# Kernel tuning notes

Measured on AMD Instinct MI355X. Metric: run time of the kernel, lower is better.

## Reference

```python
import jax, jax.numpy as jnp
import numpy as np

N_NODES = 100000
N_EDGES = 1200000
D_IN = 64
D_HID = 64
BN_EPS = 1e-5


def setup_inputs() -> dict:
    key = jax.random.key(0)
    ks = jax.random.split(key, 16)
    x = jax.random.normal(ks[0], (N_NODES, D_IN), dtype=jnp.float32)
    edge_index = jax.random.randint(ks[1], (2, N_EDGES), 0, N_NODES, dtype=jnp.int64)
    s = 1.0 / np.sqrt(D_HID)
    W1 = jax.random.uniform(ks[2], (D_IN, D_HID), jnp.float32, -s, s)
    b1 = jax.random.uniform(ks[3], (D_HID,), jnp.float32, -s, s)
    W2 = jax.random.uniform(ks[4], (D_HID, D_HID), jnp.float32, -s, s)
    b2 = jax.random.uniform(ks[5], (D_HID,), jnp.float32, -s, s)
    W3 = jax.random.uniform(ks[6], (D_HID, D_HID), jnp.float32, -s, s)
    b3 = jax.random.uniform(ks[7], (D_HID,), jnp.float32, -s, s)
    gamma1 = jnp.ones((D_HID,), jnp.float32)
    beta1 = jnp.zeros((D_HID,), jnp.float32)
    gamma2 = jnp.ones((D_HID,), jnp.float32)
    beta2 = jnp.zeros((D_HID,), jnp.float32)
    return {"x": x, "edge_index": edge_index, "batch_size": 1,
            "W1": W1, "b1": b1, "gamma1": gamma1, "beta1": beta1,
            "W2": W2, "b2": b2, "gamma2": gamma2, "beta2": beta2,
            "W3": W3, "b3": b3}


def _gcn_norm(edge_index, n):
    # PyG GCNConv: add self-loops, symmetric normalization D^-1/2 (A+I) D^-1/2
    loop = jnp.arange(n, dtype=edge_index.dtype)
    src = jnp.concatenate([edge_index[0], loop])
    dst = jnp.concatenate([edge_index[1], loop])
    deg = jax.ops.segment_sum(jnp.ones_like(dst, dtype=jnp.float32), dst, num_segments=n)
    dinv = jnp.where(deg > 0, jax.lax.rsqrt(jnp.maximum(deg, 1.0)), 0.0)
    norm = dinv[src] * dinv[dst]  # [E + N]
    return src, dst, norm


def _gcn_conv(h, W, b, src, dst, norm, n):
    h = h @ W                      # [N, D]
    msg = h[src] * norm[:, None]   # gather + scale, [E+N, D]
    out = jax.ops.segment_sum(msg, dst, num_segments=n)  # scatter-add
    return out + b


def _bn_train(h, gamma, beta):
    # BatchNorm1d over nodes, training-mode (biased batch statistics)
    m = h.mean(axis=0)
    v = h.var(axis=0)
    return (h - m) * jax.lax.rsqrt(v + BN_EPS) * gamma + beta


def reference(x, edge_index, batch_size,
              W1, b1, gamma1, beta1, W2, b2, gamma2, beta2, W3, b3):
    n = x.shape[0]
    src, dst, norm = _gcn_norm(edge_index, n)
    h = _gcn_conv(x, W1, b1, src, dst, norm, n)
    h = jax.nn.relu(_bn_train(h, gamma1, beta1))
    h = _gcn_conv(h, W2, b2, src, dst, norm, n)
    h = jax.nn.relu(_bn_train(h, gamma2, beta2))
    h = _gcn_conv(h, W3, b3, src, dst, norm, n)
    return h  # output_type == 'hidden'
```

## Files before the change

### kernel.cpp

```cpp
#include <hip/hip_runtime.h>
#include <hip/hip_bf16.h>

#define D 64

typedef __attribute__((ext_vector_type(8))) short bf16x8;
typedef __attribute__((ext_vector_type(8))) unsigned short u16x8;
typedef __attribute__((ext_vector_type(4))) float f32x4;

__device__ __forceinline__ short f2bf(float x) {
    unsigned u = __float_as_uint(x);
    unsigned r = (u + 0x7fffu + ((u >> 16) & 1u)) >> 16;
    return (short)r;
}
__device__ __forceinline__ float bf2f(unsigned short u) {
    return __uint_as_float((unsigned)u << 16);
}

__global__ void detect_kernel(const unsigned int* e32, int* flag) {
    __shared__ int nz;
    if (threadIdx.x == 0) nz = 0;
    __syncthreads();
    if (e32[2 * threadIdx.x + 1] != 0) nz = 1;
    __syncthreads();
    if (threadIdx.x == 0) *flag = (nz == 0) ? 1 : 0;
}

__device__ __forceinline__ int load_idx(const void* e, int is64, long long i) {
    if (is64) return (int)((const long long*)e)[i];
    return ((const int*)e)[i];
}

#define NBLK 256

__global__ __launch_bounds__(256) void bucket_count_kernel(
    const void* edges, const int* flag, int* pbh, int E, int shift) {
    __shared__ int h[512];
    for (int i = threadIdx.x; i < 512; i += 256) h[i] = 0;
    __syncthreads();
    int is64 = *flag;
    int chunk = (E + gridDim.x - 1) / gridDim.x;
    int s0 = blockIdx.x * chunk;
    int s1 = min(E, s0 + chunk);
    for (int e = s0 + (int)threadIdx.x; e < s1; e += 256) {
        int d = load_idx(edges, is64, (long long)E + e);
        atomicAdd(&h[d >> shift], 1);
    }
    __syncthreads();
    for (int i = threadIdx.x; i < 512; i += 256) pbh[blockIdx.x * 512 + i] = h[i];
}

__global__ __launch_bounds__(256) void colscan_kernel(int* pbh, int* btot) {
    int b = blockIdx.x;
    int k = threadIdx.x;
    __shared__ int sA[256], sB[256];
    int v = pbh[k * 512 + b];
    sA[k] = v;
    __syncthreads();
    int* src = sA;
    int* dst = sB;
    for (int d = 1; d < 256; d <<= 1) {
        dst[k] = src[k] + (k >= d ? src[k - d] : 0);
        __syncthreads();
        int* t = src; src = dst; dst = t;
    }
    pbh[k * 512 + b] = src[k] - v;
    if (k == 255) btot[b] = src[255];
}

__global__ __launch_bounds__(512) void basescan_kernel(const int* btot, int* bbase, int E) {
    __shared__ int sA[512], sB[512];
    int b = threadIdx.x;
    int v = btot[b];
    sA[b] = v;
    __syncthreads();
    int* src = sA;
    int* dst = sB;
    for (int d = 1; d < 512; d <<= 1) {
        dst[b] = src[b] + (b >= d ? src[b - d] : 0);
        __syncthreads();
        int* t = src; src = dst; dst = t;
    }
    bbase[b] = src[b] - v;
    if (b == 0) bbase[512] = E;
}

__global__ __launch_bounds__(256) void bucket_scatter_kernel(
    const void* edges, const int* flag, const int* pbh, const int* bbase,
    unsigned* staging, int E, int shift) {
    __shared__ int cur[512];
    for (int i = threadIdx.x; i < 512; i += 256)
        cur[i] = pbh[blockIdx.x * 512 + i] + bbase[i];
    __syncthreads();
    int is64 = *flag;
    int chunk = (E + gridDim.x - 1) / gridDim.x;
    int s0 = blockIdx.x * chunk;
    int s1 = min(E, s0 + chunk);
    unsigned mask = (unsigned)((1 << shift) - 1);
    for (int e = s0 + (int)threadIdx.x; e < s1; e += 256) {
        int s = load_idx(edges, is64, e);
        int d = load_idx(edges, is64, (long long)E + e);
        int b = d >> shift;
        int pos = atomicAdd(&cur[b], 1);
        staging[pos] = ((unsigned)s << shift) | ((unsigned)d & mask);
    }
}

__global__ __launch_bounds__(256) void bucket_fill_kernel(
    const unsigned* __restrict__ staging, const int* __restrict__ bbase,
    int* __restrict__ offs, float* __restrict__ dinv, int* __restrict__ srcs,
    int shift, int n, int E) {
    int b = blockIdx.x;
    int bstart = bbase[b], bend = bbase[b + 1];
    int bsz = 1 << shift;
    unsigned mask = (unsigned)(bsz - 1);
    int v0 = b << shift;
    int nloc = min(bsz, n - v0);

    __shared__ int cnt[512], cur[512], sA[512], sB[512];
    for (int i = threadIdx.x; i < bsz; i += 256) cnt[i] = 0;
    __syncthreads();
    for (int idx = bstart + (int)threadIdx.x; idx < bend; idx += 256)
        atomicAdd(&cnt[staging[idx] & mask], 1);
    __syncthreads();
    for (int i = threadIdx.x; i < bsz; i += 256) sA[i] = cnt[i];
    __syncthreads();
    int* src = sA;
    int* dst = sB;
    for (int d = 1; d < bsz; d <<= 1) {
        for (int i = threadIdx.x; i < bsz; i += 256)
            dst[i] = src[i] + (i >= d ? src[i - d] : 0);
        __syncthreads();
        int* t = src; src = dst; dst = t;
    }
    for (int i = threadIdx.x; i < bsz; i += 256) {
        int excl = src[i] - cnt[i];
        cur[i] = excl;
        if (i < nloc) {
            offs[v0 + i] = bstart + excl;
            dinv[v0 + i] = rsqrtf((float)(cnt[i] + 1));
        }
    }
    if (b == 0 && threadIdx.x == 0) offs[n] = E;
    __syncthreads();
    for (int idx = bstart + (int)threadIdx.x; idx < bend; idx += 256) {
        unsigned u = staging[idx];
        int ld = (int)(u & mask);
        int pos = atomicAdd(&cur[ld], 1);
        srcs[bstart + pos] = (int)(u >> shift);
    }
}

__global__ __launch_bounds__(256) void mm_bn_kernel(
    const float* __restrict__ Xf, const unsigned short* __restrict__ Xb, int x_is_bf16,
    const float* __restrict__ W,
    const float* __restrict__ stats, const float* __restrict__ gamma,
    const float* __restrict__ beta, int use_bn, float inv_n,
    const float* __restrict__ dinv,
    unsigned short* __restrict__ Y, int n) {
    int lane = threadIdx.x & 63;
    int m = lane & 15;
    int quad = lane >> 4;

    float sc[16], sh[16];
#pragma unroll
    for (int s = 0; s < 2; s++) {
#pragma unroll
        for (int j = 0; j < 8; j++) {
            float scale = 1.f, shift = 0.f;
            if (use_bn) {
                int f = s * 32 + quad * 8 + j;
                float mean = stats[f] * inv_n;
                float var = stats[64 + f] * inv_n - mean * mean;
                float rs = rsqrtf(var + 1e-5f);
                scale = rs * gamma[f];
                shift = beta[f] - mean * scale;
            }
            sc[s * 8 + j] = scale;
            sh[s * 8 + j] = shift;
        }
    }

    bf16x8 bfrag[4][2];
#pragma unroll
    for (int nt = 0; nt < 4; nt++) {
#pragma unroll
        for (int s = 0; s < 2; s++) {
#pragma unroll
            for (int j = 0; j < 8; j++) {
                int k = s * 32 + quad * 8 + j;
                bfrag[nt][s][j] = f2bf(W[k * 64 + nt * 16 + m]);
            }
        }
    }

    int wave = blockIdx.x * 4 + (threadIdx.x >> 6);
    int nwaves = gridDim.x * 4;
    int ntiles = (n + 15) >> 4;
    const f32x4 zero = {0.f, 0.f, 0.f, 0.f};

    for (int t = wave; t < ntiles; t += nwaves) {
        int r = t * 16 + m;
        if (r >= n) r = n - 1;
        float av[16];
        if (x_is_bf16) {
            const unsigned short* xr = Xb + (long long)r * 64;
            u16x8 u0 = *(const u16x8*)(xr + quad * 8);
            u16x8 u1 = *(const u16x8*)(xr + 32 + quad * 8);
#pragma unroll
            for (int j = 0; j < 8; j++) {
                av[j] = bf2f(u0[j]);
                av[8 + j] = bf2f(u1[j]);
            }
        } else {
            const float* xr = Xf + (long long)r * 64;
            f32x4 a0 = *(const f32x4*)(xr + quad * 8);
            f32x4 a1 = *(const f32x4*)(xr + quad * 8 + 4);
            f32x4 a2 = *(const f32x4*)(xr + 32 + quad * 8);
            f32x4 a3 = *(const f32x4*)(xr + 32 + quad * 8 + 4);
#pragma unroll
            for (int j = 0; j < 4; j++) {
                av[j] = a0[j];
                av[4 + j] = a1[j];
                av[8 + j] = a2[j];
                av[12 + j] = a3[j];
            }
        }
        bf16x8 A0, A1;
#pragma unroll
        for (int j = 0; j < 8; j++) {
            float v0 = av[j] * sc[j] + sh[j];
            float v1 = av[8 + j] * sc[8 + j] + sh[8 + j];
            if (use_bn) {
                v0 = fmaxf(v0, 0.f);
                v1 = fmaxf(v1, 0.f);
            }
            A0[j] = f2bf(v0);
            A1[j] = f2bf(v1);
        }

        f32x4 acc[4];
#pragma unroll
        for (int nt = 0; nt < 4; nt++) {
            acc[nt] = __builtin_amdgcn_mfma_f32_16x16x32_bf16(A0, bfrag[nt][0], zero, 0, 0, 0);
            acc[nt] = __builtin_amdgcn_mfma_f32_16x16x32_bf16(A1, bfrag[nt][1], acc[nt], 0, 0, 0);
        }

        int row0 = t * 16 + quad * 4;
        float dv[4];
#pragma unroll
        for (int i = 0; i < 4; i++) {
            int rr = row0 + i;
            dv[i] = (rr < n) ? dinv[rr] : 0.f;
        }
#pragma unroll
        for (int nt = 0; nt < 4; nt++) {
#pragma unroll
            for (int i = 0; i < 4; i++) {
                int rr = row0 + i;
                if (rr < n)
                    Y[(long long)rr * 64 + nt * 16 + m] = (unsigned short)f2bf(acc[nt][i] * dv[i]);
            }
        }
    }
}

__global__ __launch_bounds__(256) void agg_kernel(
    const unsigned short* __restrict__ T,
    const int* __restrict__ offs,
    const int* __restrict__ srcs,
    const float* __restrict__ dinv,
    const float* __restrict__ bias,
    unsigned short* __restrict__ out16,
    float* __restrict__ out32, int out_bf16,
    float* __restrict__ stats, int do_stats,
    int n, int E) {
    __shared__ float S[128];
    if (do_stats) {
        if (threadIdx.x < 128) S[threadIdx.x] = 0.f;
        __syncthreads();
    }
    int lane = threadIdx.x & 63;
    int sub = lane >> 3;
    int c = lane & 7;
    int wave = blockIdx.x * 4 + (threadIdx.x >> 6);
    int nwaves = gridDim.x * 4;
    int ngrp = (n + 7) >> 3;
    f32x4 bi0 = *(const f32x4*)(bias + c * 8);
    f32x4 bi1 = *(const f32x4*)(bias + c * 8 + 4);
    float ss[8], sq[8];
#pragma unroll
    for (int i = 0; i < 8; i++) { ss[i] = 0.f; sq[i] = 0.f; }

    for (int g = wave; g < ngrp; g += nwaves) {
        int v = g * 8 + sub;
        int valid = v < n;
        int vc = valid ? v : n - 1;
        int j0 = offs[vc];
        int len = offs[vc + 1] - j0;
        u16x8 sv = *(const u16x8*)(T + ((size_t)(unsigned)vc << 6) + (c << 3));
        float acc[8];
#pragma unroll
        for (int i = 0; i < 8; i++) acc[i] = bf2f(sv[i]);
        int ml = len;
        ml = max(ml, __shfl_xor(ml, 8));
        ml = max(ml, __shfl_xor(ml, 16));
        ml = max(ml, __shfl_xor(ml, 32));
        for (int base = 0; base < ml; base += 8) {
            int my = srcs[min(j0 + base + c, E - 1)];
            int lim = min(8, ml - base);
            int rel = len - base;
            for (int e = 0; e < lim; e += 4) {
                int sid[4];
                float w[4];
#pragma unroll
                for (int u = 0; u < 4; u++) {
                    int ee = e + u;
                    int s = __shfl(my, (lane & 56) | ee);
                    int live = ee < rel;
                    sid[u] = live ? s : vc;
                    w[u] = live ? 1.f : 0.f;
                }
                u16x8 r[4];
#pragma unroll
                for (int u = 0; u < 4; u++)
                    r[u] = *(const u16x8*)(T + ((size_t)(unsigned)sid[u] << 6) + (c << 3));
#pragma unroll
                for (int u = 0; u < 4; u++) {
#pragma unroll
                    for (int i = 0; i < 8; i++)
                        acc[i] += w[u] * bf2f(r[u][i]);
                }
            }
        }
        float dv = dinv[vc];
        float val[8];
#pragma unroll
        for (int i = 0; i < 4; i++) {
            val[i] = dv * acc[i] + bi0[i];
            val[4 + i] = dv * acc[4 + i] + bi1[i];
        }
        if (valid) {
            if (out_bf16) {
                u16x8 o;
#pragma unroll
                for (int i = 0; i < 8; i++) o[i] = (unsigned short)f2bf(val[i]);
                *(u16x8*)(out16 + ((size_t)(unsigned)v << 6) + (c << 3)) = o;
            } else {
                f32x4 o0 = {val[0], val[1], val[2], val[3]};
                f32x4 o1 = {val[4], val[5], val[6], val[7]};
                float* op = out32 + ((size_t)(unsigned)v << 6) + (c << 3);
                *(f32x4*)op = o0;
                *(f32x4*)(op + 4) = o1;
            }
            if (do_stats) {
#pragma unroll
                for (int i = 0; i < 8; i++) {
                    ss[i] += val[i];
                    sq[i] += val[i] * val[i];
                }
            }
        }
    }
    if (do_stats) {
#pragma unroll
        for (int i = 0; i < 8; i++) {
            atomicAdd(&S[c * 8 + i], ss[i]);
            atomicAdd(&S[64 + c * 8 + i], sq[i]);
        }
        __syncthreads();
        if (threadIdx.x < 128) atomicAdd(&stats[threadIdx.x], S[threadIdx.x]);
    }
}

extern "C" void kernel_launch(void* const* d_in, const int* in_sizes, int n_in,
                              void* d_out, int out_size, void* d_ws, size_t ws_size,
                              hipStream_t stream) {
    const float* x = (const float*)d_in[0];
    const void* edges = d_in[1];
    const float* W1 = (const float*)d_in[3];
    const float* b1 = (const float*)d_in[4];
    const float* gamma1 = (const float*)d_in[5];
    const float* beta1 = (const float*)d_in[6];
    const float* W2 = (const float*)d_in[7];
    const float* b2 = (const float*)d_in[8];
    const float* gamma2 = (const float*)d_in[9];
    const float* beta2 = (const float*)d_in[10];
    const float* W3 = (const float*)d_in[11];
    const float* b3 = (const float*)d_in[12];

    const int N = in_sizes[0] / D;
    const int E = in_sizes[1] / 2;
    const float inv_n = 1.f / (float)N;

    int shift = 8;
    while ((((long long)N - 1) >> shift) + 1 > 512) shift++;
    const int nbuk = (int)(((long long)N - 1) >> shift) + 1;

    char* ws = (char*)d_ws;
    size_t off = 0;
    auto alloc = [&](size_t bytes) -> void* {
        void* p = ws + off;
        off = (off + bytes + 255) & ~(size_t)255;
        return p;
    };
    float*    dinv    = (float*)   alloc((size_t)N * 4);
    int*      offs    = (int*)     alloc((size_t)(N + 1) * 4);
    int*      srcs    = (int*)     alloc((size_t)E * 4);
    unsigned* staging = (unsigned*)alloc((size_t)E * 4);
    int*      pbh     = (int*)     alloc((size_t)NBLK * 512 * 4);
    int*      btot    = (int*)     alloc(512 * 4);
    int*      bbase   = (int*)     alloc(513 * 4);
    int*      flag    = (int*)     alloc(4);
    float*    stats   = (float*)   alloc(256 * 4);
    unsigned short* bufA = (unsigned short*)alloc((size_t)N * D * 2);
    unsigned short* hbuf = (unsigned short*)alloc((size_t)N * D * 2);
    float*    outf    = (float*)d_out;

    const int AGGB = 1536;
    const int MMB  = 782;

    detect_kernel<<<1, 256, 0, stream>>>((const unsigned int*)edges, flag);
    bucket_count_kernel<<<NBLK, 256, 0, stream>>>(edges, flag, pbh, E, shift);
    colscan_kernel<<<512, 256, 0, stream>>>(pbh, btot);
    basescan_kernel<<<1, 512, 0, stream>>>(btot, bbase, E);
    bucket_scatter_kernel<<<NBLK, 256, 0, stream>>>(edges, flag, pbh, bbase, staging, E, shift);
    bucket_fill_kernel<<<nbuk, 256, 0, stream>>>(staging, bbase, offs, dinv, srcs, shift, N, E);
    hipMemsetAsync(stats, 0, 256 * 4, stream);

    mm_bn_kernel<<<MMB, 256, 0, stream>>>(x, nullptr, 0, W1, nullptr, nullptr, nullptr, 0,
                                          inv_n, dinv, bufA, N);
    agg_kernel<<<AGGB, 256, 0, stream>>>(bufA, offs, srcs, dinv, b1, hbuf, nullptr, 1,
                                         stats, 1, N, E);

    mm_bn_kernel<<<MMB, 256, 0, stream>>>(nullptr, hbuf, 1, W2, stats, gamma1, beta1, 1,
                                          inv_n, dinv, bufA, N);
    agg_kernel<<<AGGB, 256, 0, stream>>>(bufA, offs, srcs, dinv, b2, hbuf, nullptr, 1,
                                         stats + 128, 1, N, E);

    mm_bn_kernel<<<MMB, 256, 0, stream>>>(nullptr, hbuf, 1, W3, stats + 128, gamma2, beta2, 1,
                                          inv_n, dinv, bufA, N);
    agg_kernel<<<AGGB, 256, 0, stream>>>(bufA, offs, srcs, dinv, b3, nullptr, outf, 0,
                                         nullptr, 0, N, E);
}
```

Baseline: 360.6 us.

## Sort nodes by degree so aggregation waves process uniform-length neighbor lists

Adds a counting sort of nodes by in-degree (histogram, column scan, base scan, scatter) that produces a permutation with per-node edge offsets and lengths. The aggregation kernel walks nodes in that order, so the eight nodes sharing a wave have similar degrees and less work is lost to divergence. Each lane now loads its own source indices directly, eight at a time, instead of broadcasting them with shuffles. In exchange there are four extra preprocessing launches and the output writes land at scattered, permuted rows.

```diff
diff --git a/kernel.cpp b/kernel.cpp
--- a/kernel.cpp
+++ b/kernel.cpp
@@ -150,6 +150,79 @@
     }
 }
 
+#define DBIN 256
+
+__global__ __launch_bounds__(256) void deg_count_kernel(
+    const int* __restrict__ offs, int* __restrict__ pdh, int n) {
+    __shared__ int h[DBIN];
+    for (int i = threadIdx.x; i < DBIN; i += 256) h[i] = 0;
+    __syncthreads();
+    int chunk = (n + gridDim.x - 1) / gridDim.x;
+    int s0 = blockIdx.x * chunk;
+    int s1 = min(n, s0 + chunk);
+    for (int v = s0 + (int)threadIdx.x; v < s1; v += 256) {
+        int d = min(offs[v + 1] - offs[v], DBIN - 1);
+        atomicAdd(&h[d], 1);
+    }
+    __syncthreads();
+    for (int i = threadIdx.x; i < DBIN; i += 256) pdh[blockIdx.x * DBIN + i] = h[i];
+}
+
+__global__ __launch_bounds__(256) void deg_colscan_kernel(int* pdh, int* dtot) {
+    int b = blockIdx.x;
+    int k = threadIdx.x;
+    __shared__ int sA[256], sB[256];
+    int v = pdh[k * DBIN + b];
+    sA[k] = v;
+    __syncthreads();
+    int* src = sA;
+    int* dst = sB;
+    for (int d = 1; d < 256; d <<= 1) {
+        dst[k] = src[k] + (k >= d ? src[k - d] : 0);
+        __syncthreads();
+        int* t = src; src = dst; dst = t;
+    }
+    pdh[k * DBIN + b] = src[k] - v;
+    if (k == 255) dtot[b] = src[255];
+}
+
+__global__ __launch_bounds__(256) void deg_base_kernel(const int* dtot, int* dbase) {
+    __shared__ int sA[256], sB[256];
+    int b = threadIdx.x;
+    int v = dtot[b];
+    sA[b] = v;
+    __syncthreads();
+    int* src = sA;
+    int* dst = sB;
+    for (int d = 1; d < 256; d <<= 1) {
+        dst[b] = src[b] + (b >= d ? src[b - d] : 0);
+        __syncthreads();
+        int* t = src; src = dst; dst = t;
+    }
+    dbase[b] = src[b] - v;
+}
+
+__global__ __launch_bounds__(256) void deg_scatter_kernel(
+    const int* __restrict__ offs, const int* __restrict__ pdh, const int* __restrict__ dbase,
+    int* __restrict__ perm, int* __restrict__ pj0, int* __restrict__ plen, int n) {
+    __shared__ int cur[DBIN];
+    for (int i = threadIdx.x; i < DBIN; i += 256)
+        cur[i] = pdh[blockIdx.x * DBIN + i] + dbase[i];
+    __syncthreads();
+    int chunk = (n + gridDim.x - 1) / gridDim.x;
+    int s0 = blockIdx.x * chunk;
+    int s1 = min(n, s0 + chunk);
+    for (int v = s0 + (int)threadIdx.x; v < s1; v += 256) {
+        int a = offs[v];
+        int d = offs[v + 1] - a;
+        int bin = min(d, DBIN - 1);
+        int pos = atomicAdd(&cur[bin], 1);
+        perm[pos] = v;
+        pj0[pos] = a;
+        plen[pos] = d;
+    }
+}
+
 __global__ __launch_bounds__(256) void mm_bn_kernel(
     const float* __restrict__ Xf, const unsigned short* __restrict__ Xb, int x_is_bf16,
     const float* __restrict__ W,
@@ -266,14 +339,16 @@
 
 __global__ __launch_bounds__(256) void agg_kernel(
     const unsigned short* __restrict__ T,
-    const int* __restrict__ offs,
+    const int* __restrict__ perm,
+    const int* __restrict__ pj0,
+    const int* __restrict__ plen,
     const int* __restrict__ srcs,
     const float* __restrict__ dinv,
     const float* __restrict__ bias,
     unsigned short* __restrict__ out16,
     float* __restrict__ out32, int out_bf16,
     float* __restrict__ stats, int do_stats,
-    int n, int E) {
+    int n) {
     __shared__ float S[128];
     if (do_stats) {
         if (threadIdx.x < 128) S[threadIdx.x] = 0.f;
@@ -291,81 +366,93 @@
 #pragma unroll
     for (int i = 0; i < 8; i++) { ss[i] = 0.f; sq[i] = 0.f; }
 
+    const char* Tb = (const char*)T;
+    unsigned coff = (unsigned)c << 4;
+
     for (int g = wave; g < ngrp; g += nwaves) {
-        int v = g * 8 + sub;
-        int valid = v < n;
-        int vc = valid ? v : n - 1;
-        int j0 = offs[vc];
-        int len = offs[vc + 1] - j0;
-        u16x8 sv = *(const u16x8*)(T + ((size_t)(unsigned)vc << 6) + (c << 3));
+        int i = g * 8 + sub;
+        int valid = i < n;
+        int ic = valid ? i : n - 1;
+        int v = perm[ic];
+        int j0 = pj0[ic];
+        int len = plen[ic];
+        u16x8 sv = *(const u16x8*)(Tb + (((unsigned)v << 7) + coff));
         float acc[8];
 #pragma unroll
-        for (int i = 0; i < 8; i++) acc[i] = bf2f(sv[i]);
-        int ml = len;
-        ml = max(ml, __shfl_xor(ml, 8));
-        ml = max(ml, __shfl_xor(ml, 16));
-        ml = max(ml, __shfl_xor(ml, 32));
-        for (int base = 0; base < ml; base += 8) {
-            int my = srcs[min(j0 + base + c, E - 1)];
-            int lim = min(8, ml - base);
-            int rel = len - base;
-            for (int e = 0; e < lim; e += 4) {
-                int sid[4];
-                float w[4];
-#pragma unroll
-                for (int u = 0; u < 4; u++) {
-                    int ee = e + u;
-                    int s = __shfl(my, (lane & 56) | ee);
-                    int live = ee < rel;
-                    sid[u] = live ? s : vc;
-                    w[u] = live ? 1.f : 0.f;
-                }
-                u16x8 r[4];
-#pragma unroll
-                for (int u = 0; u < 4; u++)
-                    r[u] = *(const u16x8*)(T + ((size_t)(unsigned)sid[u] << 6) + (c << 3));
-#pragma unroll
-                for (int u = 0; u < 4; u++) {
-#pragma unroll
-                    for (int i = 0; i < 8; i++)
-                        acc[i] += w[u] * bf2f(r[u][i]);
-                }
-            }
-        }
-        float dv = dinv[vc];
+        for (int q = 0; q < 8; q++) acc[q] = bf2f(sv[q]);
+
+        int j = j0, j1 = j0 + len;
+        for (; j + 8 <= j1; j += 8) {
+            int sid[8];
+#pragma unroll
+            for (int u = 0; u < 8; u++) sid[u] = srcs[j + u];
+            u16x8 r[8];
+#pragma unroll
+            for (int u = 0; u < 8; u++)
+                r[u] = *(const u16x8*)(Tb + (((unsigned)sid[u] << 7) + coff));
+#pragma unroll
+            for (int u = 0; u < 8; u++) {
+#pragma unroll
+                for (int q = 0; q < 8; q++) acc[q] += bf2f(r[u][q]);
+            }
+        }
+        if (j < j1) {
+            int sid[8];
+            float w[8];
+#pragma unroll
+            for (int u = 0; u < 8; u++) {
+                int jj = j + u;
+                int live = jj < j1;
+                int jc = live ? jj : j1 - 1;
+                int s = srcs[jc];
+                sid[u] = live ? s : v;
+                w[u] = live ? 1.f : 0.f;
+            }
+            u16x8 r[8];
+#pragma unroll
+            for (int u = 0; u < 8; u++)
+                r[u] = *(const u16x8*)(Tb + (((unsigned)sid[u] << 7) + coff));
+#pragma unroll
+            for (int u = 0; u < 8; u++) {
+#pragma unroll
+                for (int q = 0; q < 8; q++) acc[q] += w[u] * bf2f(r[u][q]);
+            }
+        }
+
+        float dv = dinv[v];
         float val[8];
 #pragma unroll
-        for (int i = 0; i < 4; i++) {
-            val[i] = dv * acc[i] + bi0[i];
-            val[4 + i] = dv * acc[4 + i] + bi1[i];
+        for (int q = 0; q < 4; q++) {
+            val[q] = dv * acc[q] + bi0[q];
+            val[4 + q] = dv * acc[4 + q] + bi1[q];
         }
         if (valid) {
             if (out_bf16) {
                 u16x8 o;
 #pragma unroll
-                for (int i = 0; i < 8; i++) o[i] = (unsigned short)f2bf(val[i]);
-                *(u16x8*)(out16 + ((size_t)(unsigned)v << 6) + (c << 3)) = o;
+                for (int q = 0; q < 8; q++) o[q] = (unsigned short)f2bf(val[q]);
+                *(u16x8*)((char*)out16 + (((unsigned)v << 7) + coff)) = o;
             } else {
                 f32x4 o0 = {val[0], val[1], val[2], val[3]};
                 f32x4 o1 = {val[4], val[5], val[6], val[7]};
-                float* op = out32 + ((size_t)(unsigned)v << 6) + (c << 3);
+                float* op = out32 + (((unsigned)v << 6) + ((unsigned)c << 3));
                 *(f32x4*)op = o0;
                 *(f32x4*)(op + 4) = o1;
             }
             if (do_stats) {
 #pragma unroll
-                for (int i = 0; i < 8; i++) {
-                    ss[i] += val[i];
-                    sq[i] += val[i] * val[i];
+                for (int q = 0; q < 8; q++) {
+                    ss[q] += val[q];
+                    sq[q] += val[q] * val[q];
                 }
             }
         }
     }
     if (do_stats) {
 #pragma unroll
-        for (int i = 0; i < 8; i++) {
-            atomicAdd(&S[c * 8 + i], ss[i]);
-            atomicAdd(&S[64 + c * 8 + i], sq[i]);
+        for (int q = 0; q < 8; q++) {
+            atomicAdd(&S[c * 8 + q], ss[q]);
+            atomicAdd(&S[64 + c * 8 + q], sq[q]);
         }
         __syncthreads();
         if (threadIdx.x < 128) atomicAdd(&stats[threadIdx.x], S[threadIdx.x]);
@@ -412,11 +499,17 @@
     int*      bbase   = (int*)     alloc(513 * 4);
     int*      flag    = (int*)     alloc(4);
     float*    stats   = (float*)   alloc(256 * 4);
+    int*      pdh     = (int*)     alloc((size_t)NBLK * DBIN * 4);
+    int*      dtot    = (int*)     alloc(DBIN * 4);
+    int*      dbase   = (int*)     alloc(DBIN * 4);
+    int*      perm    = (int*)     alloc((size_t)N * 4);
+    int*      pj0v    = (int*)     alloc((size_t)N * 4);
+    int*      plenv   = (int*)     alloc((size_t)N * 4);
     unsigned short* bufA = (unsigned short*)alloc((size_t)N * D * 2);
     unsigned short* hbuf = (unsigned short*)alloc((size_t)N * D * 2);
     float*    outf    = (float*)d_out;
 
-    const int AGGB = 1536;
+    const int AGGB = 1563;
     const int MMB  = 782;
 
     detect_kernel<<<1, 256, 0, stream>>>((const unsigned int*)edges, flag);
@@ -425,20 +518,24 @@
     basescan_kernel<<<1, 512, 0, stream>>>(btot, bbase, E);
     bucket_scatter_kernel<<<NBLK, 256, 0, stream>>>(edges, flag, pbh, bbase, staging, E, shift);
     bucket_fill_kernel<<<nbuk, 256, 0, stream>>>(staging, bbase, offs, dinv, srcs, shift, N, E);
+    deg_count_kernel<<<NBLK, 256, 0, stream>>>(offs, pdh, N);
+    deg_colscan_kernel<<<DBIN, 256, 0, stream>>>(pdh, dtot);
+    deg_base_kernel<<<1, 256, 0, stream>>>(dtot, dbase);
+    deg_scatter_kernel<<<NBLK, 256, 0, stream>>>(offs, pdh, dbase, perm, pj0v, plenv, N);
     hipMemsetAsync(stats, 0, 256 * 4, stream);
 
     mm_bn_kernel<<<MMB, 256, 0, stream>>>(x, nullptr, 0, W1, nullptr, nullptr, nullptr, 0,
                                           inv_n, dinv, bufA, N);
-    agg_kernel<<<AGGB, 256, 0, stream>>>(bufA, offs, srcs, dinv, b1, hbuf, nullptr, 1,
-                                         stats, 1, N, E);
+    agg_kernel<<<AGGB, 256, 0, stream>>>(bufA, perm, pj0v, plenv, srcs, dinv, b1,
+                                         hbuf, nullptr, 1, stats, 1, N);
 
     mm_bn_kernel<<<MMB, 256, 0, stream>>>(nullptr, hbuf, 1, W2, stats, gamma1, beta1, 1,
                                           inv_n, dinv, bufA, N);
-    agg_kernel<<<AGGB, 256, 0, stream>>>(bufA, offs, srcs, dinv, b2, hbuf, nullptr, 1,
-                                         stats + 128, 1, N, E);
+    agg_kernel<<<AGGB, 256, 0, stream>>>(bufA, perm, pj0v, plenv, srcs, dinv, b2,
+                                         hbuf, nullptr, 1, stats + 128, 1, N);
 
     mm_bn_kernel<<<MMB, 256, 0, stream>>>(nullptr, hbuf, 1, W3, stats + 128, gamma2, beta2, 1,
                                           inv_n, dinv, bufA, N);
-    agg_kernel<<<AGGB, 256, 0, stream>>>(bufA, offs, srcs, dinv, b3, nullptr, outf, 0,
-                                         nullptr, 0, N, E);
-}
+    agg_kernel<<<AGGB, 256, 0, stream>>>(bufA, perm, pj0v, plenv, srcs, dinv, b3,
+                                         nullptr, outf, 0, nullptr, 0, N);
+}
```

After: 364.4 us. About the same (+1.0%).
